# Optimization experiments

Hardware: AMD Instinct MI355X
Metric: run time of the kernel (lower is better)

## Reference

```python
import jax, jax.numpy as jnp
import numpy as np

EPS = 1e-7
PROJ_EPS = 1e-5
MAX_TANH_ARG = 15.0
COMBINE_RELS_WEIGHT = 0.1


def _norm(x):
    return jnp.sqrt(jnp.sum(x * x, axis=-1, keepdims=True))


def log_map_zero(x):
    n = _norm(x)
    nc = jnp.clip(n, EPS, 1.0 - PROJ_EPS)
    return jnp.arctanh(nc) * x / jnp.maximum(n, EPS)


def exp_map_zero(v):
    n = jnp.maximum(_norm(v), EPS)
    return jnp.tanh(jnp.minimum(n, MAX_TANH_ARG)) * v / n


def hyperbolic_projection(x):
    n = jnp.maximum(_norm(x), EPS)
    maxnorm = 1.0 - PROJ_EPS
    return x * jnp.minimum(1.0, maxnorm / n)


def mobius_addition(u, v):
    uv = jnp.sum(u * v, axis=-1, keepdims=True)
    u2 = jnp.sum(u * u, axis=-1, keepdims=True)
    v2 = jnp.sum(v * v, axis=-1, keepdims=True)
    num = (1.0 + 2.0 * uv + v2) * u + (1.0 - u2) * v
    den = 1.0 + 2.0 * uv + u2 * v2
    return num / jnp.maximum(den, EPS)


def setup_inputs() -> dict:
    key = jax.random.key(0)
    ks = jax.random.split(key, 9)
    N, R, D, E = 50000, 1000, 128, 640000
    # embeddings start well inside the Poincare ball
    ents = 0.01 * jax.random.normal(ks[0], (N, D), dtype=jnp.float32)
    rels = 0.01 * jax.random.normal(ks[1], (R, D), dtype=jnp.float32)
    W_ent = jax.random.normal(ks[2], (D, D), dtype=jnp.float32) * (1.0 / np.sqrt(D))
    bias_vec = jnp.zeros((1, D), dtype=jnp.float32)
    ent_row = jax.random.randint(ks[3], (E,), 0, N, dtype=jnp.int32)
    ent_col = jax.random.randint(ks[4], (E,), 0, N, dtype=jnp.int32)
    rel_row = jax.random.randint(ks[5], (E,), 0, N, dtype=jnp.int32)
    rel_val = jax.random.randint(ks[6], (E,), 0, R, dtype=jnp.int32)
    near_rels_num = (1.0 + jax.random.randint(ks[7], (N,), 0, 32, dtype=jnp.int32)).astype(jnp.float32)
    return {"ents_embed_input": ents, "rels_embed_input": rels, "W_ent": W_ent,
            "bias_vec": bias_vec, "ent_row": ent_row, "ent_col": ent_col,
            "rel_row": rel_row, "rel_val": rel_val, "near_rels_num": near_rels_num}


def reference(ents_embed_input, rels_embed_input, W_ent, bias_vec,
              ent_row, ent_col, rel_row, rel_val, near_rels_num):
    N = ents_embed_input.shape[0]
    # tangent-space map + linear transform
    ents_tan = log_map_zero(ents_embed_input)          # [N, D]
    h = ents_tan @ W_ent                                # [N, D]
    # GAT-style sparse attention on adjacency (scores are detached in original)
    hd = jax.lax.stop_gradient(h)
    scores = jnp.sum(hd[ent_row] * hd[ent_col], axis=-1)  # [E]
    m = jax.ops.segment_max(scores, ent_row, num_segments=N)
    e = jnp.exp(scores - m[ent_row])
    denom = jax.ops.segment_sum(e, ent_row, num_segments=N)
    alpha = e / jnp.maximum(denom[ent_row], EPS)           # [E]
    near_ents = jax.ops.segment_sum(alpha[:, None] * h[ent_col], ent_row, num_segments=N)
    # relation neighborhood mean (gather + scatter-sum)
    edge_emb = rels_embed_input[rel_val]                   # [E, D]
    near_rels = jax.ops.segment_sum(edge_emb, rel_row, num_segments=N)
    near_rels = near_rels / near_rels_num[:, None]
    out = hyperbolic_projection(exp_map_zero(near_ents + COMBINE_RELS_WEIGHT * near_rels))
    b = hyperbolic_projection(exp_map_zero(bias_vec))
    out = hyperbolic_projection(mobius_addition(out, b))
    return out
```

## Files before the change

### kernel.cpp

```cpp
#include <hip/hip_runtime.h>
#include <hip/hip_fp16.h>
#include <math.h>

#define EPS 1e-7f
#define PROJ_EPS 1e-5f
#define MAXNORM (1.0f - PROJ_EPS)
#define D_DIM 128
#define CAP 48
#define PSHIFT 7
#define NPART 392
#define PCAP 2048
#define CHUNK 4096
#define NCONV 32
#define ATS 136
#define WTS 136
#define PREP_SMEM (64 * 132 * 4)
#define MID_SMEM (64 * ATS * 2 + 128 * WTS * 2 + 256)

typedef _Float16 f16;
typedef __attribute__((ext_vector_type(4))) _Float16 f16x4;
typedef __attribute__((ext_vector_type(8))) _Float16 f16x8;
typedef __attribute__((ext_vector_type(4))) float f32x4;

__device__ inline float wred(float v) {
    #pragma unroll
    for (int o = 32; o; o >>= 1) v += __shfl_xor(v, o, 64);
    return v;
}
__device__ inline float gred(float v) {
    v += __shfl_xor(v, 1, 64);
    v += __shfl_xor(v, 2, 64);
    v += __shfl_xor(v, 4, 64);
    v += __shfl_xor(v, 8, 64);
    return v;
}
__device__ inline void gred2(float& a, float& b) {
    a += __shfl_xor(a, 1, 64);  b += __shfl_xor(b, 1, 64);
    a += __shfl_xor(a, 2, 64);  b += __shfl_xor(b, 2, 64);
    a += __shfl_xor(a, 4, 64);  b += __shfl_xor(b, 4, 64);
    a += __shfl_xor(a, 8, 64);  b += __shfl_xor(b, 8, 64);
}
__device__ inline __half2 bc_h2(unsigned int u) { return *(__half2*)&u; }
__device__ inline unsigned int bc_u32(__half2 h) { return *(unsigned int*)&h; }

typedef _Float16 h2v __attribute__((ext_vector_type(2)));
__device__ inline h2v as_h2v(unsigned int u) { union { unsigned int u; h2v h; } c; c.u = u; return c.h; }

__device__ inline float dot8d(uint4 a, uint4 v) {
#if __has_builtin(__builtin_amdgcn_fdot2)
    float s = __builtin_amdgcn_fdot2(as_h2v(a.x), as_h2v(v.x), 0.f, false);
    s = __builtin_amdgcn_fdot2(as_h2v(a.y), as_h2v(v.y), s, false);
    s = __builtin_amdgcn_fdot2(as_h2v(a.z), as_h2v(v.z), s, false);
    s = __builtin_amdgcn_fdot2(as_h2v(a.w), as_h2v(v.w), s, false);
    return s;
#else
    __half2 t = __hmul2(bc_h2(a.x), bc_h2(v.x));
    t = __hfma2(bc_h2(a.y), bc_h2(v.y), t);
    t = __hfma2(bc_h2(a.z), bc_h2(v.z), t);
    t = __hfma2(bc_h2(a.w), bc_h2(v.w), t);
    return __low2float(t) + __high2float(t);
#endif
}
__device__ inline void acc8h(__half2* A, float w, uint4 v) {
    __half2 w2 = __float2half2_rn(w);
    A[0] = __hfma2(w2, bc_h2(v.x), A[0]);
    A[1] = __hfma2(w2, bc_h2(v.y), A[1]);
    A[2] = __hfma2(w2, bc_h2(v.z), A[2]);
    A[3] = __hfma2(w2, bc_h2(v.w), A[3]);
}
__device__ inline void add8h(__half2* A, uint4 v) {
    A[0] = __hadd2(A[0], bc_h2(v.x));
    A[1] = __hadd2(A[1], bc_h2(v.y));
    A[2] = __hadd2(A[2], bc_h2(v.z));
    A[3] = __hadd2(A[3], bc_h2(v.w));
}

__global__ __launch_bounds__(256) void k_prep(
    const float* __restrict__ W, f16* __restrict__ Wt_h,
    const int* __restrict__ er, const int* __restrict__ ec,
    const int* __restrict__ rr, const int* __restrict__ rv,
    int* __restrict__ part_e, int* __restrict__ part_r,
    int* __restrict__ cursors,
    const float* __restrict__ bias, float* __restrict__ bws,
    const float* __restrict__ rels, f16* __restrict__ rels_h, int relsN4,
    int E, int nChunk) {
    __shared__ alignas(16) unsigned char smem[PREP_SMEM];
    int tid = threadIdx.x;
    int bid = blockIdx.x;

    if (bid == 0) {
        if (tid < 64) {
            int l = tid;
            float2 bv = ((const float2*)bias)[l];
            float bn = fmaxf(sqrtf(wred(bv.x * bv.x + bv.y * bv.y)), EPS);
            float gb = tanhf(fminf(bn, 15.f)) / bn;
            float bx = gb * bv.x, by = gb * bv.y;
            float nb = fmaxf(sqrtf(wred(bx * bx + by * by)), EPS);
            float pb = fminf(1.f, MAXNORM / nb);
            bx *= pb; by *= pb;
            ((float2*)bws)[l] = make_float2(bx, by);
            float v2 = wred(bx * bx + by * by);
            if (l == 0) bws[128] = v2;
        }
        return;
    }

    if (bid == 1) {
        float* lts = (float*)smem;
        unsigned int* wt_u = (unsigned int*)Wt_h;
        for (int pass = 0; pass < 2; pass++) {
            #pragma unroll
            for (int i = 0; i < 8; i++) {
                int flat = (tid + i * 256) * 4;
                int kr = flat >> 7, cc = flat & 127;
                float4 x = *(const float4*)(W + (size_t)(pass * 64 + kr) * D_DIM + cc);
                *(float4*)&lts[kr * 132 + cc] = x;
            }
            __syncthreads();
            #pragma unroll
            for (int i = 0; i < 16; i++) {
                int flat2 = tid + i * 256;
                int c = flat2 >> 5, kp = flat2 & 31;
                float lo = lts[(2 * kp) * 132 + c];
                float hi = lts[(2 * kp + 1) * 132 + c];
                wt_u[c * 64 + pass * 32 + kp] = bc_u32(__float22half2_rn(make_float2(lo, hi)));
            }
            __syncthreads();
        }
        return;
    }

    if (bid < 2 + NCONV) {
        int gtid = (bid - 2) * 256 + tid;
        for (int i = gtid; i < relsN4; i += NCONV * 256) {
            float4 x = ((const float4*)rels)[i];
            uint2 u;
            u.x = bc_u32(__float22half2_rn(make_float2(x.x, x.y)));
            u.y = bc_u32(__float22half2_rn(make_float2(x.z, x.w)));
            ((uint2*)rels_h)[i] = u;
        }
        return;
    }

    int pid = bid - 2 - NCONV;
    int pair = (pid >= nChunk) ? 1 : 0;
    int chunk = pair ? pid - nChunk : pid;
    int* hist = (int*)smem;
    int* dlt  = hist + NPART;
    int* sc   = dlt + NPART;
    int* st   = sc + 256;
    const int* rsrc = pair ? rr : er;
    const int* psrc = pair ? rv : ec;
    int* part = pair ? part_r : part_e;
    int* cur  = cursors + pair * NPART;
    int e0 = chunk * CHUNK;
    int n = min(CHUNK, E - e0);

    for (int i = tid; i < NPART; i += 256) hist[i] = 0;
    __syncthreads();

    int myr[16], rk[16];
    #pragma unroll
    for (int i = 0; i < 16; i++) {
        int e = e0 + tid + i * 256;
        if (e < E) {
            int r = rsrc[e];
            myr[i] = r;
            rk[i] = atomicAdd(&hist[r >> PSHIFT], 1);
        } else myr[i] = -1;
    }
    __syncthreads();

    int h0 = (2 * tid < NPART) ? hist[2 * tid] : 0;
    int h1 = (2 * tid + 1 < NPART) ? hist[2 * tid + 1] : 0;
    int s = h0 + h1;
    sc[tid] = s;
    __syncthreads();
    for (int off = 1; off < 256; off <<= 1) {
        int v = (tid >= off) ? sc[tid - off] : 0;
        __syncthreads();
        sc[tid] += v;
        __syncthreads();
    }
    int excl = sc[tid] - s;
    if (2 * tid < NPART) dlt[2 * tid] = excl;
    if (2 * tid + 1 < NPART) dlt[2 * tid + 1] = excl + h0;
    __syncthreads();

    #pragma unroll
    for (int i = 0; i < 16; i++) {
        if (myr[i] >= 0) {
            int e = e0 + tid + i * 256;
            unsigned int pk = ((unsigned int)myr[i] << 16) | (unsigned int)(psrc[e] & 0xFFFF);
            st[dlt[myr[i] >> PSHIFT] + rk[i]] = (int)pk;
        }
    }
    __syncthreads();

    for (int p = tid; p < NPART; p += 256) {
        int len = hist[p];
        if (len > 0) {
            int g = atomicAdd(&cur[p], len);
            if (g + len > PCAP) g = PCAP - len;
            if (g < 0) g = 0;
            dlt[p] = p * PCAP + g - dlt[p];
        }
    }
    __syncthreads();

    for (int i = tid; i < n; i += 256) {
        unsigned int v = (unsigned int)st[i];
        int p = (int)(v >> 16) >> PSHIFT;
        part[dlt[p] + i] = (int)v;
    }
}

__global__ __launch_bounds__(256) void k_mid(
    const float* __restrict__ ents, const f16* __restrict__ Wt_h,
    __half* __restrict__ hh,
    const int* __restrict__ part_e, const int* __restrict__ part_r,
    const int* __restrict__ cursors,
    unsigned short* __restrict__ pay_e, unsigned short* __restrict__ pay_r,
    int* __restrict__ cnt, int N, int nGemm) {
    __shared__ alignas(16) unsigned char smem[MID_SMEM];
    int tid = threadIdx.x;
    int bid = blockIdx.x;

    if (bid < nGemm) {
        f16* atile = (f16*)smem;
        f16* wtile = (f16*)(smem + 64 * ATS * 2);
        float* fac = (float*)(smem + 64 * ATS * 2 + 128 * WTS * 2);
        int lane = tid & 63;
        int wv = tid >> 6;
        int r0 = bid * 64;

        #pragma unroll
        for (int i = 0; i < 8; i++) {
            int flat = (tid + i * 256) * 4;
            int rr2 = flat >> 7, cc = flat & 127;
            float4 x = make_float4(0.f, 0.f, 0.f, 0.f);
            if (r0 + rr2 < N) x = *(const float4*)(ents + (size_t)(r0 + rr2) * D_DIM + cc);
            f16x4 v4 = {(f16)x.x, (f16)x.y, (f16)x.z, (f16)x.w};
            *(f16x4*)&atile[rr2 * ATS + cc] = v4;
            float s = x.x * x.x + x.y * x.y + x.z * x.z + x.w * x.w;
            s += __shfl_xor(s, 1, 64);
            s += __shfl_xor(s, 2, 64);
            s += __shfl_xor(s, 4, 64);
            s += __shfl_xor(s, 8, 64);
            s += __shfl_xor(s, 16, 64);
            if ((lane & 31) == 0) fac[rr2] = s;
        }
        #pragma unroll
        for (int i = 0; i < 8; i++) {
            int flat4 = tid + i * 256;
            int c = flat4 >> 4, off = (flat4 & 15) * 8;
            uint4 u = ((const uint4*)Wt_h)[flat4];
            *(uint4*)&wtile[c * WTS + off] = u;
        }
        __syncthreads();

        if (tid < 64) {
            float n = sqrtf(fac[tid]);
            float ncl = fminf(fmaxf(n, EPS), MAXNORM);
            float at = 0.5f * logf((1.f + ncl) / (1.f - ncl));
            fac[tid] = at / fmaxf(n, EPS);
        }
        __syncthreads();

        int l15 = lane & 15, kseg = lane >> 4;
        int arow = wv * 16 + l15;

        f32x4 acc[8];
        #pragma unroll
        for (int ct = 0; ct < 8; ct++) acc[ct] = (f32x4){0.f, 0.f, 0.f, 0.f};

        #pragma unroll
        for (int ks = 0; ks < 4; ks++) {
            int k0 = ks * 32 + kseg * 8;
            f16x8 af = *(const f16x8*)&atile[arow * ATS + k0];
            #pragma unroll
            for (int ct = 0; ct < 8; ct++) {
                f16x8 bf = *(const f16x8*)&wtile[(ct * 16 + l15) * WTS + k0];
                acc[ct] = __builtin_amdgcn_mfma_f32_16x16x32_f16(af, bf, acc[ct], 0, 0, 0);
            }
        }
        __syncthreads();

        #pragma unroll
        for (int rg = 0; rg < 4; rg++) {
            int m = wv * 16 + kseg * 4 + rg;
            float fc = fac[m];
            #pragma unroll
            for (int ct = 0; ct < 8; ct++) {
                atile[m * ATS + ct * 16 + l15] = (f16)(acc[ct][rg] * fc);
            }
        }
        __syncthreads();

        #pragma unroll
        for (int i = 0; i < 4; i++) {
            int flat4 = tid + i * 256;
            int rr2 = flat4 >> 4, off = (flat4 & 15) * 8;
            if (r0 + rr2 < N) {
                uint4 u = *(const uint4*)&atile[rr2 * ATS + off];
                *(uint4*)((char*)hh + ((size_t)(r0 + rr2)) * 256 + off * 2) = u;
            }
        }
        return;
    }

    int b2 = bid - nGemm;
    int pair = (b2 >= NPART) ? 1 : 0;
    int p = pair ? b2 - NPART : b2;
    int* bcnt = (int*)smem;
    unsigned short* bb = (unsigned short*)(smem + 512);
    const int* part = (pair ? part_r : part_e) + (size_t)p * PCAP;
    unsigned short* pay = pair ? pay_r : pay_e;
    int* cnt_out = cnt + (size_t)pair * N;
    int n = min(cursors[pair * NPART + p], PCAP);

    if (tid < 128) bcnt[tid] = 0;
    __syncthreads();

    for (int i = tid; i < n; i += 256) {
        unsigned int v = (unsigned int)part[i];
        int rl = (int)((v >> 16) & 127);
        int slot = atomicAdd(&bcnt[rl], 1);
        if (slot < CAP) bb[rl * CAP + slot] = (unsigned short)(v & 0xFFFF);
    }
    __syncthreads();

    int rbase = p * 128;
    uint4* gdst = (uint4*)(pay + (size_t)rbase * CAP);
    const uint4* gsrc = (const uint4*)bb;
    for (int i = tid; i < 768; i += 256) gdst[i] = gsrc[i];
    if (tid < 128 && rbase + tid < N) cnt_out[rbase + tid] = bcnt[tid];
}

__global__ __launch_bounds__(256) void k_row(
    const __half* __restrict__ hh, const __half* __restrict__ rels_h,
    const float* __restrict__ bws, const float* __restrict__ nrn,
    const int* __restrict__ cnt, const unsigned short* __restrict__ pay_e,
    const unsigned short* __restrict__ pay_r,
    float* __restrict__ out, int N) {
    int wv = threadIdx.x >> 6, lane = threadIdx.x & 63;
    int sub = lane >> 4, sl = lane & 15;
    int gb = lane & 48;
    int r = blockIdx.x * 16 + wv * 4 + sub;
    bool valid = r < N;
    int rc = valid ? r : 0;

    const char* hB = (const char*)hh + sl * 16;
    const char* rB = (const char*)rels_h + sl * 16;
    uint4 hraw = *(const uint4*)(hB + ((size_t)rc << 8));

    int deg  = valid ? min(cnt[rc], CAP) : 0;
    int degr = valid ? min(cnt[N + rc], CAP) : 0;

    size_t be = (size_t)rc * CAP;
    int i0e = (sl      < deg) ? (int)pay_e[be + sl]      : 0;
    int i1e = (sl + 16 < deg) ? (int)pay_e[be + sl + 16] : 0;
    int i2e = (sl + 32 < deg) ? (int)pay_e[be + sl + 32] : 0;
    int i0r = (sl      < degr) ? (int)pay_r[be + sl]      : 0;
    int i1r = (sl + 16 < degr) ? (int)pay_r[be + sl + 16] : 0;
    int i2r = (sl + 32 < degr) ? (int)pay_r[be + sl + 32] : 0;

    int md = deg;
    md = max(md, __shfl_xor(md, 16, 64));
    md = max(md, __shfl_xor(md, 32, 64));
    int mdr = degr;
    mdr = max(mdr, __shfl_xor(mdr, 16, 64));
    mdr = max(mdr, __shfl_xor(mdr, 32, 64));

    __half2 aA[4] = {bc_h2(0u), bc_h2(0u), bc_h2(0u), bc_h2(0u)};
    float den = 0.f;

    auto att1 = [&](int idxreg, int k, int t) {
        int c = __shfl(idxreg, gb | k);
        uint4 v = *(const uint4*)(hB + ((size_t)c << 8));
        float s = gred(dot8d(hraw, v));
        float w = (t < deg) ? __expf(s) : 0.f;
        den += w;
        acc8h(aA, w, v);
    };
    auto att2 = [&](int idxreg, int k, int t) {
        int c0 = __shfl(idxreg, gb | k);
        int c1 = __shfl(idxreg, gb | (k + 1));
        uint4 v0 = *(const uint4*)(hB + ((size_t)c0 << 8));
        uint4 v1 = *(const uint4*)(hB + ((size_t)c1 << 8));
        float s0 = dot8d(hraw, v0);
        float s1 = dot8d(hraw, v1);
        gred2(s0, s1);
        float w0 = (t < deg) ? __expf(s0) : 0.f;
        float w1 = (t + 1 < deg) ? __expf(s1) : 0.f;
        den += w0 + w1;
        acc8h(aA, w0, v0);
        acc8h(aA, w1, v1);
    };

    {
        int l0 = min(md, 16);
        int k = 0;
        for (; k + 2 <= l0; k += 2) att2(i0e, k, k);
        if (k < l0) att1(i0e, k, k);
        if (md > 16) {
            int l1 = min(md - 16, 16);
            for (k = 0; k + 2 <= l1; k += 2) att2(i1e, k, 16 + k);
            if (k < l1) att1(i1e, k, 16 + k);
            if (md > 32) {
                int l2 = min(md - 32, 16);
                for (k = 0; k + 2 <= l2; k += 2) att2(i2e, k, 32 + k);
                if (k < l2) att1(i2e, k, 32 + k);
            }
        }
    }

    __half2 rA[4] = {bc_h2(0u), bc_h2(0u), bc_h2(0u), bc_h2(0u)};
    auto rel1 = [&](int idxreg, int k, int t) {
        int id = __shfl(idxreg, gb | k);
        uint4 v = *(const uint4*)(rB + ((size_t)id << 8));
        if (t < degr) add8h(rA, v);
    };
    auto rel2 = [&](int idxreg, int k, int t) {
        int id0 = __shfl(idxreg, gb | k);
        int id1 = __shfl(idxreg, gb | (k + 1));
        uint4 v0 = *(const uint4*)(rB + ((size_t)id0 << 8));
        uint4 v1 = *(const uint4*)(rB + ((size_t)id1 << 8));
        if (t < degr) add8h(rA, v0);
        if (t + 1 < degr) add8h(rA, v1);
    };
    {
        int l0 = min(mdr, 16);
        int k = 0;
        for (; k + 2 <= l0; k += 2) rel2(i0r, k, k);
        if (k < l0) rel1(i0r, k, k);
        if (mdr > 16) {
            int l1 = min(mdr - 16, 16);
            for (k = 0; k + 2 <= l1; k += 2) rel2(i1r, k, 16 + k);
            if (k < l1) rel1(i1r, k, 16 + k);
            if (mdr > 32) {
                int l2 = min(mdr - 32, 16);
                for (k = 0; k + 2 <= l2; k += 2) rel2(i2r, k, 32 + k);
                if (k < l2) rel1(i2r, k, 32 + k);
            }
        }
    }

    float inv  = 1.f / fmaxf(den, EPS);
    float innr = 0.1f / nrn[rc];
    float2 a0 = __half22float2(aA[0]), a1 = __half22float2(aA[1]);
    float2 a2 = __half22float2(aA[2]), a3 = __half22float2(aA[3]);
    float2 r0f = __half22float2(rA[0]), r1f = __half22float2(rA[1]);
    float2 r2f = __half22float2(rA[2]), r3f = __half22float2(rA[3]);
    float v0 = a0.x * inv + r0f.x * innr, v1 = a0.y * inv + r0f.y * innr;
    float v2_ = a1.x * inv + r1f.x * innr, v3 = a1.y * inv + r1f.y * innr;
    float v4 = a2.x * inv + r2f.x * innr, v5 = a2.y * inv + r2f.y * innr;
    float v6 = a3.x * inv + r3f.x * innr, v7 = a3.y * inv + r3f.y * innr;

    float pn = v0*v0 + v1*v1 + v2_*v2_ + v3*v3 + v4*v4 + v5*v5 + v6*v6 + v7*v7;
    pn = gred(pn);
    float sq = sqrtf(pn);
    float nn = fmaxf(sq, EPS);
    float tt = __expf(2.f * fminf(nn, 15.f));
    float g = (tt - 1.f) / ((tt + 1.f) * nn);
    float n2 = fmaxf(g * sq, EPS);
    float pf = fminf(1.f, MAXNORM / n2);
    float gp = g * pf;
    float o0 = gp*v0, o1 = gp*v1, o2 = gp*v2_, o3 = gp*v3;
    float o4 = gp*v4, o5 = gp*v5, o6 = gp*v6, o7 = gp*v7;
    float un = n2 * pf;
    float u2 = un * un;

    const float4* bp = (const float4*)(bws + sl * 8);
    float4 b0 = bp[0], b1 = bp[1];
    float bv2 = bws[128];
    float puv = o0*b0.x + o1*b0.y + o2*b0.z + o3*b0.w
              + o4*b1.x + o5*b1.y + o6*b1.z + o7*b1.w;
    puv = gred(puv);
    float ca = 1.f + 2.f * puv + bv2;
    float cb = 1.f - u2;
    float idm = 1.f / fmaxf(1.f + 2.f * puv + u2 * bv2, EPS);
    float x0 = (ca*o0 + cb*b0.x) * idm, x1 = (ca*o1 + cb*b0.y) * idm;
    float x2 = (ca*o2 + cb*b0.z) * idm, x3 = (ca*o3 + cb*b0.w) * idm;
    float x4 = (ca*o4 + cb*b1.x) * idm, x5 = (ca*o5 + cb*b1.y) * idm;
    float x6 = (ca*o6 + cb*b1.z) * idm, x7 = (ca*o7 + cb*b1.w) * idm;
    float pr = x0*x0 + x1*x1 + x2*x2 + x3*x3 + x4*x4 + x5*x5 + x6*x6 + x7*x7;
    pr = gred(pr);
    float n3 = fmaxf(sqrtf(pr), EPS);
    float pf3 = fminf(1.f, MAXNORM / n3);

    if (valid) {
        float4* op = (float4*)(out + (size_t)r * D_DIM + sl * 8);
        op[0] = make_float4(x0 * pf3, x1 * pf3, x2 * pf3, x3 * pf3);
        op[1] = make_float4(x4 * pf3, x5 * pf3, x6 * pf3, x7 * pf3);
    }
}

extern "C" void kernel_launch(void* const* d_in, const int* in_sizes, int n_in,
                              void* d_out, int out_size, void* d_ws, size_t ws_size,
                              hipStream_t stream) {
    const float* ents = (const float*)d_in[0];
    const float* rels = (const float*)d_in[1];
    const float* W    = (const float*)d_in[2];
    const float* bias = (const float*)d_in[3];
    const int* er = (const int*)d_in[4];
    const int* ec = (const int*)d_in[5];
    const int* rr = (const int*)d_in[6];
    const int* rv = (const int*)d_in[7];
    const float* nrn = (const float*)d_in[8];
    int N = in_sizes[0] / D_DIM;
    int R = in_sizes[1] / D_DIM;
    int E = in_sizes[4];
    float* out = (float*)d_out;

    char* p = (char*)d_ws;
    auto alloc = [&](size_t bytes) {
        char* q = p;
        p += (bytes + 255) & ~(size_t)255;
        return q;
    };
    const int PADN = NPART * 128;
    __half* hh     = (__half*)alloc((size_t)N * D_DIM * 2);
    f16* rels_h    = (f16*)alloc((size_t)R * D_DIM * 2);
    f16* Wt_h      = (f16*)alloc((size_t)D_DIM * D_DIM * 2);
    int* cnt    = (int*)alloc((size_t)2 * N * 4);
    unsigned short* pay_e = (unsigned short*)alloc((size_t)PADN * CAP * 2);
    unsigned short* pay_r = (unsigned short*)alloc((size_t)PADN * CAP * 2);
    int* part_e = (int*)alloc((size_t)NPART * PCAP * 4);
    int* part_r = (int*)alloc((size_t)NPART * PCAP * 4);
    int* cursors = (int*)alloc((size_t)2 * NPART * 4);
    float* bws   = (float*)alloc((size_t)132 * 4);

    hipMemsetAsync(cursors, 0, (size_t)2 * NPART * 4, stream);

    int nGemm = (N + 63) / 64;
    int nChunk = (E + CHUNK - 1) / CHUNK;
    int relsN4 = R * D_DIM / 4;

    k_prep<<<2 + NCONV + 2 * nChunk, 256, 0, stream>>>(
        W, Wt_h, er, ec, rr, rv, part_e, part_r, cursors, bias, bws,
        rels, rels_h, relsN4, E, nChunk);

    k_mid<<<nGemm + 2 * NPART, 256, 0, stream>>>(
        ents, Wt_h, hh, part_e, part_r, cursors, pay_e, pay_r, cnt, N, nGemm);

    k_row<<<(N + 15) / 16, 256, 0, stream>>>(
        hh, (const __half*)rels_h, bws, nrn, cnt, pay_e, pay_r, out, N);
}
```

Measured before the change: 81.21 us.

## Restructure launches so edge partitioning runs concurrently with the GEMM

The work is regrouped across kernels. A tiny pre-kernel now zeroes the cursors, computes the bias and transposes W. One main kernel runs the GEMM blocks, the relation fp16 conversion and the edge-partitioning chunks together, and a separate bucket kernel follows. This replaces the memset call and lets the partitioning overlap with the GEMM instead of running in an earlier serial kernel. It adds one kernel launch, and the small two-block pre-kernel now sits serially in front of everything.

```diff
diff --git a/kernel.cpp b/kernel.cpp
--- a/kernel.cpp
+++ b/kernel.cpp
@@ -14,8 +14,8 @@
 #define NCONV 32
 #define ATS 136
 #define WTS 136
-#define PREP_SMEM (64 * 132 * 4)
-#define MID_SMEM (64 * ATS * 2 + 128 * WTS * 2 + 256)
+#define PRE0_SMEM (64 * 132 * 4)
+#define MAIN_SMEM (64 * ATS * 2 + 128 * WTS * 2 + 256)
 
 typedef _Float16 f16;
 typedef __attribute__((ext_vector_type(4))) _Float16 f16x4;
@@ -75,20 +75,15 @@
     A[3] = __hadd2(A[3], bc_h2(v.w));
 }
 
-__global__ __launch_bounds__(256) void k_prep(
+__global__ __launch_bounds__(256) void k_pre0(
     const float* __restrict__ W, f16* __restrict__ Wt_h,
-    const int* __restrict__ er, const int* __restrict__ ec,
-    const int* __restrict__ rr, const int* __restrict__ rv,
-    int* __restrict__ part_e, int* __restrict__ part_r,
-    int* __restrict__ cursors,
     const float* __restrict__ bias, float* __restrict__ bws,
-    const float* __restrict__ rels, f16* __restrict__ rels_h, int relsN4,
-    int E, int nChunk) {
-    __shared__ alignas(16) unsigned char smem[PREP_SMEM];
+    int* __restrict__ cursors) {
+    __shared__ alignas(16) unsigned char smem[PRE0_SMEM];
     int tid = threadIdx.x;
-    int bid = blockIdx.x;
-
-    if (bid == 0) {
+
+    if (blockIdx.x == 0) {
+        for (int i = tid; i < 2 * NPART; i += 256) cursors[i] = 0;
         if (tid < 64) {
             int l = tid;
             float2 bv = ((const float2*)bias)[l];
@@ -105,124 +100,39 @@
         return;
     }
 
-    if (bid == 1) {
-        float* lts = (float*)smem;
-        unsigned int* wt_u = (unsigned int*)Wt_h;
-        for (int pass = 0; pass < 2; pass++) {
-            #pragma unroll
-            for (int i = 0; i < 8; i++) {
-                int flat = (tid + i * 256) * 4;
-                int kr = flat >> 7, cc = flat & 127;
-                float4 x = *(const float4*)(W + (size_t)(pass * 64 + kr) * D_DIM + cc);
-                *(float4*)&lts[kr * 132 + cc] = x;
-            }
-            __syncthreads();
-            #pragma unroll
-            for (int i = 0; i < 16; i++) {
-                int flat2 = tid + i * 256;
-                int c = flat2 >> 5, kp = flat2 & 31;
-                float lo = lts[(2 * kp) * 132 + c];
-                float hi = lts[(2 * kp + 1) * 132 + c];
-                wt_u[c * 64 + pass * 32 + kp] = bc_u32(__float22half2_rn(make_float2(lo, hi)));
-            }
-            __syncthreads();
-        }
-        return;
-    }
-
-    if (bid < 2 + NCONV) {
-        int gtid = (bid - 2) * 256 + tid;
-        for (int i = gtid; i < relsN4; i += NCONV * 256) {
-            float4 x = ((const float4*)rels)[i];
-            uint2 u;
-            u.x = bc_u32(__float22half2_rn(make_float2(x.x, x.y)));
-            u.y = bc_u32(__float22half2_rn(make_float2(x.z, x.w)));
-            ((uint2*)rels_h)[i] = u;
-        }
-        return;
-    }
-
-    int pid = bid - 2 - NCONV;
-    int pair = (pid >= nChunk) ? 1 : 0;
-    int chunk = pair ? pid - nChunk : pid;
-    int* hist = (int*)smem;
-    int* dlt  = hist + NPART;
-    int* sc   = dlt + NPART;
-    int* st   = sc + 256;
-    const int* rsrc = pair ? rr : er;
-    const int* psrc = pair ? rv : ec;
-    int* part = pair ? part_r : part_e;
-    int* cur  = cursors + pair * NPART;
-    int e0 = chunk * CHUNK;
-    int n = min(CHUNK, E - e0);
-
-    for (int i = tid; i < NPART; i += 256) hist[i] = 0;
-    __syncthreads();
-
-    int myr[16], rk[16];
-    #pragma unroll
-    for (int i = 0; i < 16; i++) {
-        int e = e0 + tid + i * 256;
-        if (e < E) {
-            int r = rsrc[e];
-            myr[i] = r;
-            rk[i] = atomicAdd(&hist[r >> PSHIFT], 1);
-        } else myr[i] = -1;
-    }
-    __syncthreads();
-
-    int h0 = (2 * tid < NPART) ? hist[2 * tid] : 0;
-    int h1 = (2 * tid + 1 < NPART) ? hist[2 * tid + 1] : 0;
-    int s = h0 + h1;
-    sc[tid] = s;
-    __syncthreads();
-    for (int off = 1; off < 256; off <<= 1) {
-        int v = (tid >= off) ? sc[tid - off] : 0;
-        __syncthreads();
-        sc[tid] += v;
-        __syncthreads();
-    }
-    int excl = sc[tid] - s;
-    if (2 * tid < NPART) dlt[2 * tid] = excl;
-    if (2 * tid + 1 < NPART) dlt[2 * tid + 1] = excl + h0;
-    __syncthreads();
-
-    #pragma unroll
-    for (int i = 0; i < 16; i++) {
-        if (myr[i] >= 0) {
-            int e = e0 + tid + i * 256;
-            unsigned int pk = ((unsigned int)myr[i] << 16) | (unsigned int)(psrc[e] & 0xFFFF);
-            st[dlt[myr[i] >> PSHIFT] + rk[i]] = (int)pk;
-        }
-    }
-    __syncthreads();
-
-    for (int p = tid; p < NPART; p += 256) {
-        int len = hist[p];
-        if (len > 0) {
-            int g = atomicAdd(&cur[p], len);
-            if (g + len > PCAP) g = PCAP - len;
-            if (g < 0) g = 0;
-            dlt[p] = p * PCAP + g - dlt[p];
-        }
-    }
-    __syncthreads();
-
-    for (int i = tid; i < n; i += 256) {
-        unsigned int v = (unsigned int)st[i];
-        int p = (int)(v >> 16) >> PSHIFT;
-        part[dlt[p] + i] = (int)v;
-    }
-}
-
-__global__ __launch_bounds__(256) void k_mid(
+    float* lts = (float*)smem;
+    unsigned int* wt_u = (unsigned int*)Wt_h;
+    for (int pass = 0; pass < 2; pass++) {
+        #pragma unroll
+        for (int i = 0; i < 8; i++) {
+            int flat = (tid + i * 256) * 4;
+            int kr = flat >> 7, cc = flat & 127;
+            float4 x = *(const float4*)(W + (size_t)(pass * 64 + kr) * D_DIM + cc);
+            *(float4*)&lts[kr * 132 + cc] = x;
+        }
+        __syncthreads();
+        #pragma unroll
+        for (int i = 0; i < 16; i++) {
+            int flat2 = tid + i * 256;
+            int c = flat2 >> 5, kp = flat2 & 31;
+            float lo = lts[(2 * kp) * 132 + c];
+            float hi = lts[(2 * kp + 1) * 132 + c];
+            wt_u[c * 64 + pass * 32 + kp] = bc_u32(__float22half2_rn(make_float2(lo, hi)));
+        }
+        __syncthreads();
+    }
+}
+
+__global__ __launch_bounds__(256) void k_main(
     const float* __restrict__ ents, const f16* __restrict__ Wt_h,
     __half* __restrict__ hh,
-    const int* __restrict__ part_e, const int* __restrict__ part_r,
-    const int* __restrict__ cursors,
-    unsigned short* __restrict__ pay_e, unsigned short* __restrict__ pay_r,
-    int* __restrict__ cnt, int N, int nGemm) {
-    __shared__ alignas(16) unsigned char smem[MID_SMEM];
+    const int* __restrict__ er, const int* __restrict__ ec,
+    const int* __restrict__ rr, const int* __restrict__ rv,
+    int* __restrict__ part_e, int* __restrict__ part_r,
+    int* __restrict__ cursors,
+    const float* __restrict__ rels, f16* __restrict__ rels_h, int relsN4,
+    int N, int E, int nGemm, int nChunk) {
+    __shared__ alignas(16) unsigned char smem[MAIN_SMEM];
     int tid = threadIdx.x;
     int bid = blockIdx.x;
 
@@ -309,11 +219,101 @@
         return;
     }
 
-    int b2 = bid - nGemm;
-    int pair = (b2 >= NPART) ? 1 : 0;
-    int p = pair ? b2 - NPART : b2;
-    int* bcnt = (int*)smem;
-    unsigned short* bb = (unsigned short*)(smem + 512);
+    if (bid < nGemm + NCONV) {
+        int gtid = (bid - nGemm) * 256 + tid;
+        for (int i = gtid; i < relsN4; i += NCONV * 256) {
+            float4 x = ((const float4*)rels)[i];
+            uint2 u;
+            u.x = bc_u32(__float22half2_rn(make_float2(x.x, x.y)));
+            u.y = bc_u32(__float22half2_rn(make_float2(x.z, x.w)));
+            ((uint2*)rels_h)[i] = u;
+        }
+        return;
+    }
+
+    int pid = bid - nGemm - NCONV;
+    int pair = (pid >= nChunk) ? 1 : 0;
+    int chunk = pair ? pid - nChunk : pid;
+    int* hist = (int*)smem;
+    int* dlt  = hist + NPART;
+    int* sc   = dlt + NPART;
+    int* st   = sc + 256;
+    const int* rsrc = pair ? rr : er;
+    const int* psrc = pair ? rv : ec;
+    int* part = pair ? part_r : part_e;
+    int* cur  = cursors + pair * NPART;
+    int e0 = chunk * CHUNK;
+    int n = min(CHUNK, E - e0);
+
+    for (int i = tid; i < NPART; i += 256) hist[i] = 0;
+    __syncthreads();
+
+    int myr[16], rk[16];
+    #pragma unroll
+    for (int i = 0; i < 16; i++) {
+        int e = e0 + tid + i * 256;
+        if (e < E) {
+            int r = rsrc[e];
+            myr[i] = r;
+            rk[i] = atomicAdd(&hist[r >> PSHIFT], 1);
+        } else myr[i] = -1;
+    }
+    __syncthreads();
+
+    int h0 = (2 * tid < NPART) ? hist[2 * tid] : 0;
+    int h1 = (2 * tid + 1 < NPART) ? hist[2 * tid + 1] : 0;
+    int s = h0 + h1;
+    sc[tid] = s;
+    __syncthreads();
+    for (int off = 1; off < 256; off <<= 1) {
+        int v = (tid >= off) ? sc[tid - off] : 0;
+        __syncthreads();
+        sc[tid] += v;
+        __syncthreads();
+    }
+    int excl = sc[tid] - s;
+    if (2 * tid < NPART) dlt[2 * tid] = excl;
+    if (2 * tid + 1 < NPART) dlt[2 * tid + 1] = excl + h0;
+    __syncthreads();
+
+    #pragma unroll
+    for (int i = 0; i < 16; i++) {
+        if (myr[i] >= 0) {
+            int e = e0 + tid + i * 256;
+            unsigned int pk = ((unsigned int)myr[i] << 16) | (unsigned int)(psrc[e] & 0xFFFF);
+            st[dlt[myr[i] >> PSHIFT] + rk[i]] = (int)pk;
+        }
+    }
+    __syncthreads();
+
+    for (int p = tid; p < NPART; p += 256) {
+        int len = hist[p];
+        if (len > 0) {
+            int g = atomicAdd(&cur[p], len);
+            if (g + len > PCAP) g = PCAP - len;
+            if (g < 0) g = 0;
+            dlt[p] = p * PCAP + g - dlt[p];
+        }
+    }
+    __syncthreads();
+
+    for (int i = tid; i < n; i += 256) {
+        unsigned int v = (unsigned int)st[i];
+        int p = (int)(v >> 16) >> PSHIFT;
+        part[dlt[p] + i] = (int)v;
+    }
+}
+
+__global__ __launch_bounds__(256) void k_bucket(
+    const int* __restrict__ part_e, const int* __restrict__ part_r,
+    const int* __restrict__ cursors,
+    unsigned short* __restrict__ pay_e, unsigned short* __restrict__ pay_r,
+    int* __restrict__ cnt, int N) {
+    __shared__ int bcnt[128];
+    __shared__ unsigned short bb[128 * CAP];
+    int tid = threadIdx.x;
+    int p = blockIdx.x;
+    int pair = blockIdx.y;
     const int* part = (pair ? part_r : part_e) + (size_t)p * PCAP;
     unsigned short* pay = pair ? pay_r : pay_e;
     int* cnt_out = cnt + (size_t)pair * N;
@@ -531,18 +531,17 @@
     int* cursors = (int*)alloc((size_t)2 * NPART * 4);
     float* bws   = (float*)alloc((size_t)132 * 4);
 
-    hipMemsetAsync(cursors, 0, (size_t)2 * NPART * 4, stream);
-
     int nGemm = (N + 63) / 64;
     int nChunk = (E + CHUNK - 1) / CHUNK;
     int relsN4 = R * D_DIM / 4;
 
-    k_prep<<<2 + NCONV + 2 * nChunk, 256, 0, stream>>>(
-        W, Wt_h, er, ec, rr, rv, part_e, part_r, cursors, bias, bws,
-        rels, rels_h, relsN4, E, nChunk);
-
-    k_mid<<<nGemm + 2 * NPART, 256, 0, stream>>>(
-        ents, Wt_h, hh, part_e, part_r, cursors, pay_e, pay_r, cnt, N, nGemm);
+    k_pre0<<<2, 256, 0, stream>>>(W, Wt_h, bias, bws, cursors);
+
+    k_main<<<nGemm + NCONV + 2 * nChunk, 256, 0, stream>>>(
+        ents, Wt_h, hh, er, ec, rr, rv, part_e, part_r, cursors,
+        rels, rels_h, relsN4, N, E, nGemm, nChunk);
+
+    k_bucket<<<dim3(NPART, 2), 256, 0, stream>>>(part_e, part_r, cursors, pay_e, pay_r, cnt, N);
 
     k_row<<<(N + 15) / 16, 256, 0, stream>>>(
         hh, (const __half*)rels_h, bws, nrn, cnt, pay_e, pay_r, out, N);
```

New measurement: 78.56 us. 3.3% less time.
